# Kernel optimization log

Hardware: AMD Instinct MI355X
Metric: run time of the kernel (lower is better)

## Reference

```python
import jax, jax.numpy as jnp
import numpy as np

B, IN_DIM, D, C = 16384, 1024, 256, 100


def setup_inputs() -> dict:
    key = jax.random.key(0)
    k1, k2, k3, k4 = jax.random.split(key, 4)
    x = jax.random.normal(k1, (B, IN_DIM), dtype=jnp.float32)
    W = jax.random.normal(k2, (IN_DIM, D), dtype=jnp.float32) * (1.0 / np.sqrt(IN_DIM))
    b = jax.random.normal(k3, (D,), dtype=jnp.float32) * 0.01
    P = jax.random.normal(k4, (C, D), dtype=jnp.float32)  # class prototypes [C, D]
    return {"x": x, "W": W, "b": b, "P": P}


def reference(x, W, b, P):
    # Encoder: Z = x @ W + b  -> [B, D]
    Z = x @ W + b
    d = Z.shape[-1]
    # MSE(r, p) = mean((r - p)^2) = (|r|^2 - 2 r.p + |p|^2) / D
    # Computed via expansion to avoid the [B, C, D] broadcast intermediate.
    sq = (
        jnp.sum(Z * Z, axis=-1, keepdims=True)      # [B, 1]
        - 2.0 * (Z @ P.T)                            # [B, C]
        + jnp.sum(P * P, axis=-1)[None, :]           # [1, C]
    )
    return -sq / d  # [B, C]
```

## Files before the change

kernel.cpp:

```cpp
#include <hip/hip_runtime.h>

#define BATCH 16384
#define KDIM  1024
#define DDIM  256
#define CNUM  100
#define CPAD  112

typedef __bf16 bf16x8 __attribute__((ext_vector_type(8)));
typedef float  floatx4 __attribute__((ext_vector_type(4)));

static __device__ __forceinline__ unsigned short f2b(float f) {
    return __builtin_bit_cast(unsigned short, (__bf16)f);
}

__global__ __launch_bounds__(256) void prep(const float* __restrict__ W,
                                            const float* __restrict__ P,
                                            unsigned short* __restrict__ Wt2,
                                            unsigned short* __restrict__ Pbf,
                                            float* __restrict__ pnorm2) {
    __shared__ float T[32][33];
    const int bid = blockIdx.x;
    if (bid < 256) {
        const int k0 = (bid & 31) * 32;
        const int n0 = (bid >> 5) * 32;
        const int j  = threadIdx.x & 31;
        const int i0 = threadIdx.x >> 5;
#pragma unroll
        for (int l = 0; l < 4; ++l) {
            int i = i0 + l * 8;
            T[i][j] = W[(k0 + i) * DDIM + n0 + j];
        }
        __syncthreads();
        if (threadIdx.x < 128) {
            const int l  = threadIdx.x & 63;
            const int fn = threadIdx.x >> 6;
            const int lm = l & 15, lq = l >> 4;
            bf16x8 v;
#pragma unroll
            for (int jj = 0; jj < 8; ++jj)
                v[jj] = (__bf16)T[lq * 8 + jj][fn * 16 + lm];
            const int nblk = (n0 >> 4) + fn;
            const int kblk = k0 >> 5;
            *(bf16x8*)&Wt2[(nblk * 32 + kblk) * 512 + l * 8] = v;
        }
    } else {
        const int wave = threadIdx.x >> 6;
        const int lane = threadIdx.x & 63;
        const int c = (bid - 256) * 4 + wave;
        float s = 0.f;
#pragma unroll
        for (int jj = 0; jj < 4; ++jj) {
            int d = jj * 64 + lane;
            float v = (c < CNUM) ? P[c * DDIM + d] : 0.f;
            Pbf[c * DDIM + d] = f2b(v);
            s += v * v;
        }
#pragma unroll
        for (int m = 1; m < 64; m <<= 1) s += __shfl_xor(s, m, 64);
        if (lane == 0) pnorm2[c] = s;
    }
}

#define KSTEP(KK, CUR, NXT)                                                    \
    {                                                                          \
        unsigned short* As_c = U + (CUR) * 2048;                               \
        const int kb_ = (KK) >> 5;                                             \
        if ((KK) + 64 < KDIM) {                                                \
            _Pragma("unroll")                                                  \
            for (int kf = 0; kf < 2; ++kf) {                                   \
                _Pragma("unroll")                                              \
                for (int f = 0; f < 4; ++f)                                    \
                    b[NXT][kf][f] = *(const bf16x8*)(gB + f * 16384 +          \
                                                     (kb_ + 2 + kf) * 512);    \
            }                                                                  \
            bf16x8 ha;                                                         \
            ha[0] = (__bf16)pa0[0]; ha[1] = (__bf16)pa0[1];                    \
            ha[2] = (__bf16)pa0[2]; ha[3] = (__bf16)pa0[3];                    \
            ha[4] = (__bf16)pa1[0]; ha[5] = (__bf16)pa1[1];                    \
            ha[6] = (__bf16)pa1[2]; ha[7] = (__bf16)pa1[3];                    \
            *(bf16x8*)&(U + (NXT) * 2048)[ldsA] = ha;                          \
            if ((KK) + 128 < KDIM) {                                           \
                pa0 = *(const floatx4*)(gA + (KK) + 128);                      \
                pa1 = *(const floatx4*)(gA + (KK) + 132);                      \
            }                                                                  \
        }                                                                      \
        _Pragma("unroll")                                                      \
        for (int kf = 0; kf < 2; ++kf) {                                       \
            const int sw = kf ? sw1 : sw0;                                     \
            bf16x8 a0 = *(const bf16x8*)&As_c[lm * 64 + sw];                   \
            bf16x8 a1 = *(const bf16x8*)&As_c[(16 + lm) * 64 + sw];            \
            _Pragma("unroll")                                                  \
            for (int f = 0; f < 4; ++f) {                                      \
                acc[0][f] = __builtin_amdgcn_mfma_f32_16x16x32_bf16(           \
                    a0, b[CUR][kf][f], acc[0][f], 0, 0, 0);                    \
                acc[1][f] = __builtin_amdgcn_mfma_f32_16x16x32_bf16(           \
                    a1, b[CUR][kf][f], acc[1][f], 0, 0, 0);                    \
            }                                                                  \
        }                                                                      \
        asm volatile("s_waitcnt lgkmcnt(0)\n\ts_barrier" ::: "memory");        \
    }

__global__ __launch_bounds__(256, 2) void fused_main(
    const float* __restrict__ x, const float* __restrict__ bias,
    const unsigned short* __restrict__ Wt2, const unsigned short* __restrict__ Pbf,
    const float* __restrict__ pnorm2, float* __restrict__ out)
{
    __shared__ unsigned short U[8448];
    __shared__ float rn2[4][32];
    unsigned short* Zs = U;

    const int tid  = threadIdx.x;
    const int wave = tid >> 6;
    const int lane = tid & 63;
    const int lm   = lane & 15;
    const int lq   = lane >> 4;
    const int r0   = blockIdx.x * 32;

    const int rowA = tid >> 3;
    const int kbA  = tid & 7;
    const float* gA = x + (r0 + rowA) * KDIM + kbA * 8;
    const int ldsA = rowA * 64 + ((kbA ^ (rowA & 7)) * 8);

    const unsigned short* gB = Wt2 + wave * 4 * 16384 + lane * 8;

    const int sw0 = ((0 * 4 + lq) ^ (lm & 7)) * 8;
    const int sw1 = ((1 * 4 + lq) ^ (lm & 7)) * 8;

    floatx4 acc[2][4];
#pragma unroll
    for (int g = 0; g < 2; ++g)
#pragma unroll
        for (int f = 0; f < 4; ++f) { acc[g][f][0]=0.f; acc[g][f][1]=0.f; acc[g][f][2]=0.f; acc[g][f][3]=0.f; }

    bf16x8 b[2][2][4];

    {
        floatx4 q0 = *(const floatx4*)(gA);
        floatx4 q1 = *(const floatx4*)(gA + 4);
        bf16x8 ha;
        ha[0] = (__bf16)q0[0]; ha[1] = (__bf16)q0[1];
        ha[2] = (__bf16)q0[2]; ha[3] = (__bf16)q0[3];
        ha[4] = (__bf16)q1[0]; ha[5] = (__bf16)q1[1];
        ha[6] = (__bf16)q1[2]; ha[7] = (__bf16)q1[3];
        *(bf16x8*)&U[ldsA] = ha;
    }
#pragma unroll
    for (int kf = 0; kf < 2; ++kf)
#pragma unroll
        for (int f = 0; f < 4; ++f)
            b[0][kf][f] = *(const bf16x8*)(gB + f * 16384 + kf * 512);
    floatx4 pa0 = *(const floatx4*)(gA + 64);
    floatx4 pa1 = *(const floatx4*)(gA + 68);
    asm volatile("s_waitcnt lgkmcnt(0)\n\ts_barrier" ::: "memory");

    for (int kk0 = 0; kk0 < KDIM; kk0 += 128) {
        KSTEP(kk0, 0, 1)
        KSTEP(kk0 + 64, 1, 0)
    }

#pragma unroll
    for (int f = 0; f < 4; ++f) {
        float bb = bias[wave * 64 + f * 16 + lm];
#pragma unroll
        for (int g = 0; g < 2; ++g)
#pragma unroll
            for (int r = 0; r < 4; ++r) acc[g][f][r] += bb;
    }

#pragma unroll
    for (int g = 0; g < 2; ++g) {
        float s0 = 0.f, s1 = 0.f, s2 = 0.f, s3 = 0.f;
#pragma unroll
        for (int f = 0; f < 4; ++f) {
            s0 += acc[g][f][0] * acc[g][f][0];
            s1 += acc[g][f][1] * acc[g][f][1];
            s2 += acc[g][f][2] * acc[g][f][2];
            s3 += acc[g][f][3] * acc[g][f][3];
        }
#pragma unroll
        for (int m = 1; m < 16; m <<= 1) {
            s0 += __shfl_xor(s0, m, 64);
            s1 += __shfl_xor(s1, m, 64);
            s2 += __shfl_xor(s2, m, 64);
            s3 += __shfl_xor(s3, m, 64);
        }
        if (lm == 0) {
            int rl = g * 16 + lq * 4;
            rn2[wave][rl + 0] = s0;
            rn2[wave][rl + 1] = s1;
            rn2[wave][rl + 2] = s2;
            rn2[wave][rl + 3] = s3;
        }
    }

#pragma unroll
    for (int g = 0; g < 2; ++g)
#pragma unroll
        for (int f = 0; f < 4; ++f) {
            int col = wave * 64 + f * 16 + lm;
#pragma unroll
            for (int r = 0; r < 4; ++r)
                Zs[(g * 16 + lq * 4 + r) * 264 + col] = f2b(acc[g][f][r]);
        }
    __syncthreads();

#pragma unroll
    for (int t = 0; t < 2; ++t) {
        const int ct = wave * 2 + t;
        if (ct < 7) {
            floatx4 acc2[2];
#pragma unroll
            for (int nf = 0; nf < 2; ++nf) { acc2[nf][0]=0.f; acc2[nf][1]=0.f; acc2[nf][2]=0.f; acc2[nf][3]=0.f; }
            const unsigned short* gP = Pbf + (ct * 16 + lm) * DDIM + lq * 8;
#pragma unroll
            for (int ks = 0; ks < 8; ++ks) {
                bf16x8 ap = *(const bf16x8*)(gP + ks * 32);
#pragma unroll
                for (int nf = 0; nf < 2; ++nf) {
                    bf16x8 bz = *(const bf16x8*)&Zs[(nf * 16 + lm) * 264 + ks * 32 + lq * 8];
                    acc2[nf] = __builtin_amdgcn_mfma_f32_16x16x32_bf16(ap, bz, acc2[nf], 0, 0, 0);
                }
            }
            int c0 = ct * 16 + lq * 4;
            if (c0 < CNUM) {
                floatx4 pn = *(const floatx4*)(pnorm2 + c0);
#pragma unroll
                for (int nf = 0; nf < 2; ++nf) {
                    int rl = nf * 16 + lm;
                    float rn = rn2[0][rl] + rn2[1][rl] + rn2[2][rl] + rn2[3][rl];
                    floatx4 o;
#pragma unroll
                    for (int r = 0; r < 4; ++r)
                        o[r] = (2.f * acc2[nf][r] - rn - pn[r]) * (1.f / 256.f);
                    *(floatx4*)&out[(r0 + rl) * CNUM + c0] = o;
                }
            }
        }
    }
}

extern "C" void kernel_launch(void* const* d_in, const int* in_sizes, int n_in,
                              void* d_out, int out_size, void* d_ws, size_t ws_size,
                              hipStream_t stream) {
    const float* x = (const float*)d_in[0];
    const float* W = (const float*)d_in[1];
    const float* b = (const float*)d_in[2];
    const float* P = (const float*)d_in[3];
    float* out = (float*)d_out;

    unsigned short* Wt2 = (unsigned short*)d_ws;
    unsigned short* Pbf = Wt2 + KDIM * DDIM;
    float* pn2 = (float*)(Pbf + CPAD * DDIM);

    prep<<<256 + CPAD / 4, 256, 0, stream>>>(W, P, Wt2, Pbf, pn2);
    fused_main<<<BATCH / 32, 256, 0, stream>>>(x, b, Wt2, Pbf, pn2, out);
}
```

Measured before the change: 116.1 us.

## Load A operands straight from global into registers, drop LDS staging, 64-row tiles

The encoder GEMM no longer converts x into LDS and reads it back. Each wave loads its fp32 A fragments directly into registers, double-buffered, and converts them to bf16 in-register, so the per-k-step barriers go away. The row tile grows from 32 to 64 per block, which halves the grid and lowers the occupancy hint to 1. In exchange, all four waves redundantly fetch the same x rows from global/L1, register pressure rises sharply, and there are fewer resident waves to hide memory latency.

```diff
diff --git a/kernel.cpp b/kernel.cpp
--- a/kernel.cpp
+++ b/kernel.cpp
@@ -61,114 +61,106 @@
     }
 }
 
-#define KSTEP(KK, CUR, NXT)                                                    \
+#define KBODY(KK, QC, BCr, QN, BN)                                             \
     {                                                                          \
-        unsigned short* As_c = U + (CUR) * 2048;                               \
         const int kb_ = (KK) >> 5;                                             \
+                     \
         if ((KK) + 64 < KDIM) {                                                \
+            _Pragma("unroll")                                                  \
+            for (int i = 0; i < 8; ++i) {                                      \
+                const int g = i & 3, kf = i >> 2;                              \
+                QN[2 * i]     = *(const floatx4*)(gAr[g] + (KK) + 64 + kf * 32);     \
+                QN[2 * i + 1] = *(const floatx4*)(gAr[g] + (KK) + 64 + kf * 32 + 4); \
+            }                                                                  \
             _Pragma("unroll")                                                  \
             for (int kf = 0; kf < 2; ++kf) {                                   \
                 _Pragma("unroll")                                              \
                 for (int f = 0; f < 4; ++f)                                    \
-                    b[NXT][kf][f] = *(const bf16x8*)(gB + f * 16384 +          \
-                                                     (kb_ + 2 + kf) * 512);    \
-            }                                                                  \
-            bf16x8 ha;                                                         \
-            ha[0] = (__bf16)pa0[0]; ha[1] = (__bf16)pa0[1];                    \
-            ha[2] = (__bf16)pa0[2]; ha[3] = (__bf16)pa0[3];                    \
-            ha[4] = (__bf16)pa1[0]; ha[5] = (__bf16)pa1[1];                    \
-            ha[6] = (__bf16)pa1[2]; ha[7] = (__bf16)pa1[3];                    \
-            *(bf16x8*)&(U + (NXT) * 2048)[ldsA] = ha;                          \
-            if ((KK) + 128 < KDIM) {                                           \
-                pa0 = *(const floatx4*)(gA + (KK) + 128);                      \
-                pa1 = *(const floatx4*)(gA + (KK) + 132);                      \
+                    BN[kf * 4 + f] = *(const bf16x8*)(gB + f * 16384 +         \
+                                                      (kb_ + 2 + kf) * 512);   \
+            }                                                                  \
+        }                                                                      \
+           \
+        bf16x8 af[8];                                                          \
+        _Pragma("unroll")                                                      \
+        for (int i = 0; i < 8; ++i) {                                          \
+            _Pragma("unroll")                                                  \
+            for (int j = 0; j < 4; ++j) {                                      \
+                af[i][j]     = (__bf16)QC[2 * i][j];                           \
+                af[i][4 + j] = (__bf16)QC[2 * i + 1][j];                       \
             }                                                                  \
         }                                                                      \
         _Pragma("unroll")                                                      \
         for (int kf = 0; kf < 2; ++kf) {                                       \
-            const int sw = kf ? sw1 : sw0;                                     \
-            bf16x8 a0 = *(const bf16x8*)&As_c[lm * 64 + sw];                   \
-            bf16x8 a1 = *(const bf16x8*)&As_c[(16 + lm) * 64 + sw];            \
             _Pragma("unroll")                                                  \
             for (int f = 0; f < 4; ++f) {                                      \
-                acc[0][f] = __builtin_amdgcn_mfma_f32_16x16x32_bf16(           \
-                    a0, b[CUR][kf][f], acc[0][f], 0, 0, 0);                    \
-                acc[1][f] = __builtin_amdgcn_mfma_f32_16x16x32_bf16(           \
-                    a1, b[CUR][kf][f], acc[1][f], 0, 0, 0);                    \
+                _Pragma("unroll")                                              \
+                for (int g = 0; g < 4; ++g)                                    \
+                    acc[g][f] = __builtin_amdgcn_mfma_f32_16x16x32_bf16(       \
+                        af[kf * 4 + g], BCr[kf * 4 + f], acc[g][f], 0, 0, 0);  \
             }                                                                  \
         }                                                                      \
-        asm volatile("s_waitcnt lgkmcnt(0)\n\ts_barrier" ::: "memory");        \
-    }
-
-__global__ __launch_bounds__(256, 2) void fused_main(
+    }
+
+__global__ __launch_bounds__(256, 1) void fused_main(
     const float* __restrict__ x, const float* __restrict__ bias,
     const unsigned short* __restrict__ Wt2, const unsigned short* __restrict__ Pbf,
     const float* __restrict__ pnorm2, float* __restrict__ out)
 {
-    __shared__ unsigned short U[8448];
-    __shared__ float rn2[4][32];
-    unsigned short* Zs = U;
+    __shared__ unsigned short Zs[16896];
+    __shared__ float rn2[4][64];
 
     const int tid  = threadIdx.x;
     const int wave = tid >> 6;
     const int lane = tid & 63;
     const int lm   = lane & 15;
     const int lq   = lane >> 4;
-    const int r0   = blockIdx.x * 32;
-
-    const int rowA = tid >> 3;
-    const int kbA  = tid & 7;
-    const float* gA = x + (r0 + rowA) * KDIM + kbA * 8;
-    const int ldsA = rowA * 64 + ((kbA ^ (rowA & 7)) * 8);
+    const int r0   = blockIdx.x * 64;
+
+    const float* gAr[4];
+#pragma unroll
+    for (int g = 0; g < 4; ++g)
+        gAr[g] = x + (size_t)(r0 + g * 16 + lm) * KDIM + lq * 8;
 
     const unsigned short* gB = Wt2 + wave * 4 * 16384 + lane * 8;
 
-    const int sw0 = ((0 * 4 + lq) ^ (lm & 7)) * 8;
-    const int sw1 = ((1 * 4 + lq) ^ (lm & 7)) * 8;
-
-    floatx4 acc[2][4];
-#pragma unroll
-    for (int g = 0; g < 2; ++g)
+    floatx4 acc[4][4];
+#pragma unroll
+    for (int g = 0; g < 4; ++g)
 #pragma unroll
         for (int f = 0; f < 4; ++f) { acc[g][f][0]=0.f; acc[g][f][1]=0.f; acc[g][f][2]=0.f; acc[g][f][3]=0.f; }
 
-    bf16x8 b[2][2][4];
-
-    {
-        floatx4 q0 = *(const floatx4*)(gA);
-        floatx4 q1 = *(const floatx4*)(gA + 4);
-        bf16x8 ha;
-        ha[0] = (__bf16)q0[0]; ha[1] = (__bf16)q0[1];
-        ha[2] = (__bf16)q0[2]; ha[3] = (__bf16)q0[3];
-        ha[4] = (__bf16)q1[0]; ha[5] = (__bf16)q1[1];
-        ha[6] = (__bf16)q1[2]; ha[7] = (__bf16)q1[3];
-        *(bf16x8*)&U[ldsA] = ha;
+    floatx4 qa[16], qb[16];
+    bf16x8  bc[8],  bn[8];
+
+#pragma unroll
+    for (int i = 0; i < 8; ++i) {
+        const int g = i & 3, kf = i >> 2;
+        qa[2 * i]     = *(const floatx4*)(gAr[g] + kf * 32);
+        qa[2 * i + 1] = *(const floatx4*)(gAr[g] + kf * 32 + 4);
     }
 #pragma unroll
     for (int kf = 0; kf < 2; ++kf)
 #pragma unroll
         for (int f = 0; f < 4; ++f)
-            b[0][kf][f] = *(const bf16x8*)(gB + f * 16384 + kf * 512);
-    floatx4 pa0 = *(const floatx4*)(gA + 64);
-    floatx4 pa1 = *(const floatx4*)(gA + 68);
-    asm volatile("s_waitcnt lgkmcnt(0)\n\ts_barrier" ::: "memory");
+            bc[kf * 4 + f] = *(const bf16x8*)(gB + f * 16384 + kf * 512);
 
     for (int kk0 = 0; kk0 < KDIM; kk0 += 128) {
-        KSTEP(kk0, 0, 1)
-        KSTEP(kk0 + 64, 1, 0)
+        KBODY(kk0,      qa, bc, qb, bn)
+        KBODY(kk0 + 64, qb, bn, qa, bc)
     }
 
 #pragma unroll
     for (int f = 0; f < 4; ++f) {
         float bb = bias[wave * 64 + f * 16 + lm];
 #pragma unroll
-        for (int g = 0; g < 2; ++g)
+        for (int g = 0; g < 4; ++g)
 #pragma unroll
             for (int r = 0; r < 4; ++r) acc[g][f][r] += bb;
     }
 
 #pragma unroll
-    for (int g = 0; g < 2; ++g) {
+    for (int g = 0; g < 4; ++g) {
         float s0 = 0.f, s1 = 0.f, s2 = 0.f, s3 = 0.f;
 #pragma unroll
         for (int f = 0; f < 4; ++f) {
@@ -194,7 +186,7 @@
     }
 
 #pragma unroll
-    for (int g = 0; g < 2; ++g)
+    for (int g = 0; g < 4; ++g)
 #pragma unroll
         for (int f = 0; f < 4; ++f) {
             int col = wave * 64 + f * 16 + lm;
@@ -208,15 +200,15 @@
     for (int t = 0; t < 2; ++t) {
         const int ct = wave * 2 + t;
         if (ct < 7) {
-            floatx4 acc2[2];
-#pragma unroll
-            for (int nf = 0; nf < 2; ++nf) { acc2[nf][0]=0.f; acc2[nf][1]=0.f; acc2[nf][2]=0.f; acc2[nf][3]=0.f; }
+            floatx4 acc2[4];
+#pragma unroll
+            for (int nf = 0; nf < 4; ++nf) { acc2[nf][0]=0.f; acc2[nf][1]=0.f; acc2[nf][2]=0.f; acc2[nf][3]=0.f; }
             const unsigned short* gP = Pbf + (ct * 16 + lm) * DDIM + lq * 8;
 #pragma unroll
             for (int ks = 0; ks < 8; ++ks) {
                 bf16x8 ap = *(const bf16x8*)(gP + ks * 32);
 #pragma unroll
-                for (int nf = 0; nf < 2; ++nf) {
+                for (int nf = 0; nf < 4; ++nf) {
                     bf16x8 bz = *(const bf16x8*)&Zs[(nf * 16 + lm) * 264 + ks * 32 + lq * 8];
                     acc2[nf] = __builtin_amdgcn_mfma_f32_16x16x32_bf16(ap, bz, acc2[nf], 0, 0, 0);
                 }
@@ -225,7 +217,7 @@
             if (c0 < CNUM) {
                 floatx4 pn = *(const floatx4*)(pnorm2 + c0);
 #pragma unroll
-                for (int nf = 0; nf < 2; ++nf) {
+                for (int nf = 0; nf < 4; ++nf) {
                     int rl = nf * 16 + lm;
                     float rn = rn2[0][rl] + rn2[1][rl] + rn2[2][rl] + rn2[3][rl];
                     floatx4 o;
@@ -253,5 +245,5 @@
     float* pn2 = (float*)(Pbf + CPAD * DDIM);
 
     prep<<<256 + CPAD / 4, 256, 0, stream>>>(W, P, Wt2, Pbf, pn2);
-    fused_main<<<BATCH / 32, 256, 0, stream>>>(x, b, Wt2, Pbf, pn2, out);
-}
+    fused_main<<<BATCH / 64, 256, 0, stream>>>(x, b, Wt2, Pbf, pn2, out);
+}
```

Result: slower. 131.2 us (+13.0%).
